# Kernel optimization log

Measured on AMD Instinct MI355X. Metric: run time of the kernel, lower is better.

The kernel has to match this reference:

```python
import jax, jax.numpy as jnp
import numpy as np

B, E, DM = 2, 1024, 512          # batch, n_edges, d_model
H, DK, DV = 8, 64, 64            # heads, d_k, d_v
MAX_NEIGHBOR = 5                 # == attn_max_dist
LN_EPS = 1e-6
NEG = -1e9


def setup_inputs() -> dict:
    key = jax.random.key(0)
    ks = jax.random.split(key, 9)
    s = 0.02
    return {
        "x": jax.random.normal(ks[0], (B, DM, E, 1), jnp.float32),
        "dist": jax.random.randint(ks[1], (B, E, E), 0, 12, jnp.int32),
        "base_rpr": jax.random.normal(ks[2], (MAX_NEIGHBOR + 1, DK), jnp.float32) * s,
        "w_q": jax.random.normal(ks[3], (DM, H * DK), jnp.float32) * s,
        "w_k": jax.random.normal(ks[4], (DM, H * DK), jnp.float32) * s,
        "w_v": jax.random.normal(ks[5], (DM, H * DV), jnp.float32) * s,
        "w_fc": jax.random.normal(ks[6], (H * DV, DM), jnp.float32) * s,
        "ln_g": jnp.ones((DM,), jnp.float32),
        "ln_b": jnp.zeros((DM,), jnp.float32),
    }


def reference(x, dist, base_rpr, w_q, w_k, w_v, w_fc, ln_g, ln_b):
    temp = jnp.asarray(DK, x.dtype) ** 0.5
    # local-attention mask (dist <= attn_max_dist); all edges valid (same-size meshes)
    mask = dist <= MAX_NEIGHBOR                      # [B,E,E] bool

    s = jnp.transpose(x[..., 0], (0, 2, 1))          # [B,E,DM]
    residual = s

    # LayerNorm applied to q only (as in the torch module)
    mu = s.mean(-1, keepdims=True)
    var = ((s - mu) ** 2).mean(-1, keepdims=True)
    qn = (s - mu) / jnp.sqrt(var + LN_EPS) * ln_g + ln_b

    q = (qn @ w_q).reshape(B, E, H, DK).transpose(0, 2, 1, 3)   # [B,H,E,DK]
    k = (s @ w_k).reshape(B, E, H, DK).transpose(0, 2, 1, 3)
    v = (s @ w_v).reshape(B, E, H, DV).transpose(0, 2, 1, 3)

    # relative-position representations gathered by (clipped) distance
    rpr = base_rpr[jnp.minimum(dist, MAX_NEIGHBOR)]  # [B,E,E,DK]

    qs = q / temp
    attn1 = jnp.einsum("bhid,bhjd->bhij", qs, k)
    attn2 = jnp.einsum("bhid,bijd->bhij", qs, rpr)
    logits = jnp.where(mask[:, None], attn1 + attn2, NEG)
    attn = jax.nn.softmax(logits, axis=-1)           # [B,H,E,E]

    out = jnp.einsum("bhij,bhjd->bhid", attn, v)     # [B,H,E,DV]
    out = out.transpose(0, 2, 1, 3).reshape(B, E, H * DV) @ w_fc + residual
    x_out = out.transpose(0, 2, 1)[..., None]        # [B,DM,E,1]

    mf = mask[:, None].astype(attn.dtype)            # [B,1,E,E]
    attn_per_edge = (attn * mf).sum((1, 2)) / mf.sum((1, 2))  # [B,E]
    return x_out, attn, attn_per_edge
```

## Files before the change

### kernel.cpp

```cpp
#include <hip/hip_runtime.h>

#define NB_B 2
#define NB_E 1024
#define NB_DM 512
#define NB_H 8
#define NEGV -1e9f

typedef __attribute__((ext_vector_type(8))) __bf16 bf16x8;
typedef __attribute__((ext_vector_type(8))) unsigned short u16x8;
typedef __attribute__((ext_vector_type(4))) float f32x4;

static __device__ __forceinline__ float bf2f(unsigned short u){
  union { unsigned int i; float f; } v; v.i = ((unsigned int)u) << 16; return v.f;
}
static __device__ __forceinline__ unsigned short f2bf(float f){
  union { float f; unsigned int i; } v; v.f = f;
  unsigned int r = v.i + 0x7FFFu + ((v.i >> 16) & 1u);
  return (unsigned short)(r >> 16);
}
static __device__ __forceinline__ f32x4 mfma16(bf16x8 a, bf16x8 b, f32x4 c){
  return __builtin_amdgcn_mfma_f32_16x16x32_bf16(a, b, c, 0, 0, 0);
}
static __device__ __forceinline__ float fast_exp2(float x){
#if __has_builtin(__builtin_amdgcn_exp2f)
  return __builtin_amdgcn_exp2f(x);
#else
  return exp2f(x);
#endif
}

__global__ void k_transpose_x(const float* __restrict__ x, unsigned short* __restrict__ s_bf){
  __shared__ float tile[32][33];
  const int b = blockIdx.z;
  const int d0 = blockIdx.y * 32;
  const int e0 = blockIdx.x * 32;
  const int tx = threadIdx.x, ty = threadIdx.y;
  #pragma unroll
  for (int r = 0; r < 4; ++r){
    const int d = d0 + ty + r*8;
    tile[ty + r*8][tx] = x[((size_t)b*NB_DM + d)*NB_E + e0 + tx];
  }
  __syncthreads();
  #pragma unroll
  for (int r = 0; r < 4; ++r){
    const int e = e0 + ty + r*8;
    s_bf[((size_t)b*NB_E + e)*NB_DM + d0 + tx] = f2bf(tile[tx][ty + r*8]);
  }
}

__global__ void k_transpose_w(const float* __restrict__ w0, const float* __restrict__ w1,
                              const float* __restrict__ w2, const float* __restrict__ w3,
                              unsigned short* __restrict__ wT){
  __shared__ float tile[32][33];
  const int which = blockIdx.z;
  const float* w = which==0 ? w0 : which==1 ? w1 : which==2 ? w2 : w3;
  unsigned short* dst = wT + (size_t)which*512*512;
  const int k0 = blockIdx.y*32, n0 = blockIdx.x*32;
  const int tx = threadIdx.x, ty = threadIdx.y;
  #pragma unroll
  for (int r = 0; r < 4; ++r)
    tile[ty + r*8][tx] = w[(size_t)(k0 + ty + r*8)*512 + n0 + tx];
  __syncthreads();
  #pragma unroll
  for (int r = 0; r < 4; ++r)
    dst[(size_t)(n0 + ty + r*8)*512 + k0 + tx] = f2bf(tile[tx][ty + r*8]);
}

__global__ __launch_bounds__(256) void k_ln(const unsigned short* __restrict__ s_bf,
    unsigned short* __restrict__ qn_bf, const float* __restrict__ gg, const float* __restrict__ bb){
  const int row = blockIdx.x*4 + (threadIdx.x >> 6);
  const int l = threadIdx.x & 63;
  const unsigned short* sp = s_bf + (size_t)row*512 + l*8;
  u16x8 v = *(const u16x8*)sp;
  float f[8]; float sum = 0.f, sq = 0.f;
  #pragma unroll
  for (int i = 0; i < 8; ++i){ f[i] = bf2f(v[i]); sum += f[i]; sq += f[i]*f[i]; }
  #pragma unroll
  for (int off = 32; off >= 1; off >>= 1){
    sum += __shfl_xor(sum, off);
    sq  += __shfl_xor(sq, off);
  }
  const float mu  = sum * (1.f/512.f);
  const float var = sq * (1.f/512.f) - mu*mu;
  const float rstd = rsqrtf(var + 1e-6f);
  const float4 g0 = *(const float4*)(gg + l*8);
  const float4 g1 = *(const float4*)(gg + l*8 + 4);
  const float4 b0 = *(const float4*)(bb + l*8);
  const float4 b1 = *(const float4*)(bb + l*8 + 4);
  const float gv[8] = {g0.x,g0.y,g0.z,g0.w,g1.x,g1.y,g1.z,g1.w};
  const float bv[8] = {b0.x,b0.y,b0.z,b0.w,b1.x,b1.y,b1.z,b1.w};
  u16x8 o;
  #pragma unroll
  for (int i = 0; i < 8; ++i) o[i] = f2bf((f[i]-mu)*rstd*gv[i] + bv[i]);
  *(u16x8*)(qn_bf + (size_t)row*512 + l*8) = o;
}

__global__ __launch_bounds__(256) void k_dist(const int* __restrict__ dist,
    unsigned char* __restrict__ d8, int* __restrict__ cnt){
  const int b = blockIdx.y;
  const int i0 = blockIdx.x * 16;
  const int t = threadIdx.x;
  int c0 = 0, c1 = 0, c2 = 0, c3 = 0;
  #pragma unroll 4
  for (int r = 0; r < 16; ++r){
    const int row = i0 + r;
    const int4 d = ((const int4*)(dist + ((size_t)b*NB_E + row)*NB_E))[t];
    uchar4 o;
    o.x = (unsigned char)(d.x <= 5 ? d.x : 6);
    o.y = (unsigned char)(d.y <= 5 ? d.y : 6);
    o.z = (unsigned char)(d.z <= 5 ? d.z : 6);
    o.w = (unsigned char)(d.w <= 5 ? d.w : 6);
    ((uchar4*)(d8 + ((size_t)b*NB_E + row)*NB_E))[t] = o;
    c0 += (d.x <= 5); c1 += (d.y <= 5); c2 += (d.z <= 5); c3 += (d.w <= 5);
  }
  int* cb = cnt + b*NB_E + t*4;
  atomicAdd(cb + 0, c0);
  atomicAdd(cb + 1, c1);
  atomicAdd(cb + 2, c2);
  atomicAdd(cb + 3, c3);
}

__global__ __launch_bounds__(256) void k_gemm_qkv(
    const unsigned short* __restrict__ qn, const unsigned short* __restrict__ s,
    const unsigned short* __restrict__ wT, const float* __restrict__ base_rpr,
    unsigned short* __restrict__ Qb, unsigned short* __restrict__ Kb,
    unsigned short* __restrict__ VTb, float* __restrict__ qr)
{
  const int z = blockIdx.z;
  const unsigned short* A  = (z == 0) ? qn : s;
  const unsigned short* BT = wT + (size_t)z*262144;
  const int tid = threadIdx.x;
  const int l = tid & 63, wv = tid >> 6;
  const int ll = l & 15, lg = l >> 4;
  const int m0 = blockIdx.x*64 + wv*16;
  const int n0 = blockIdx.y*64;
  const unsigned short* arow = A + (size_t)(m0 + ll)*512 + lg*8;
  f32x4 acc[4];
  #pragma unroll
  for (int nt = 0; nt < 4; ++nt) acc[nt] = (f32x4){0.f,0.f,0.f,0.f};
  #pragma unroll
  for (int ks = 0; ks < 16; ++ks){
    bf16x8 a = *(const bf16x8*)(arow + ks*32);
    #pragma unroll
    for (int nt = 0; nt < 4; ++nt){
      bf16x8 bv = *(const bf16x8*)(BT + (size_t)(n0 + nt*16 + ll)*512 + ks*32 + lg*8);
      acc[nt] = mfma16(a, bv, acc[nt]);
    }
  }
  const int rbase = m0 + lg*4;
  const int bidx = rbase >> 10;
  const int e = rbase & 1023;
  const int h = n0 >> 6;
  if (z == 0){
    float rprv[6][4];
    #pragma unroll
    for (int c = 0; c < 6; ++c)
      #pragma unroll
      for (int nt = 0; nt < 4; ++nt)
        rprv[c][nt] = base_rpr[c*64 + nt*16 + ll];
    #pragma unroll
    for (int nt = 0; nt < 4; ++nt){
      const int dk = nt*16 + ll;
      unsigned short* dp = Qb + (((size_t)bidx*NB_H + h)*NB_E + e)*64 + dk;
      #pragma unroll
      for (int r = 0; r < 4; ++r)
        dp[(size_t)r*64] = f2bf(acc[nt][r]*0.125f);
    }
    #pragma unroll
    for (int r = 0; r < 4; ++r){
      #pragma unroll
      for (int c = 0; c < 6; ++c){
        float tv = 0.f;
        #pragma unroll
        for (int nt = 0; nt < 4; ++nt) tv += acc[nt][r]*0.125f*rprv[c][nt];
        tv += __shfl_xor(tv, 1);
        tv += __shfl_xor(tv, 2);
        tv += __shfl_xor(tv, 4);
        tv += __shfl_xor(tv, 8);
        if (ll == 0)
          qr[(((size_t)(bidx*NB_H + h)*NB_E) + e + r)*8 + c] = tv;
      }
    }
  } else if (z == 1){
    #pragma unroll
    for (int nt = 0; nt < 4; ++nt){
      const int dk = nt*16 + ll;
      unsigned short* dp = Kb + (((size_t)bidx*NB_H + h)*NB_E + e)*64 + dk;
      #pragma unroll
      for (int r = 0; r < 4; ++r)
        dp[(size_t)r*64] = f2bf(acc[nt][r]);
    }
  } else {
    #pragma unroll
    for (int nt = 0; nt < 4; ++nt){
      const int dv = nt*16 + ll;
      ushort4 ov;
      ov.x = f2bf(acc[nt][0]); ov.y = f2bf(acc[nt][1]);
      ov.z = f2bf(acc[nt][2]); ov.w = f2bf(acc[nt][3]);
      *(ushort4*)(VTb + (((size_t)bidx*NB_H + h)*64 + dv)*NB_E + e) = ov;
    }
  }
}

__global__ __launch_bounds__(256) void k_fc(
    const unsigned short* __restrict__ A, const unsigned short* __restrict__ BT,
    float* __restrict__ dst_f, const float* __restrict__ resid)
{
  const int tid = threadIdx.x;
  const int l = tid & 63, wv = tid >> 6;
  const int ll = l & 15, lg = l >> 4;
  const int m0 = blockIdx.x*64 + wv*16;
  const int n0 = blockIdx.y*64;
  const unsigned short* arow = A + (size_t)(m0 + ll)*512 + lg*8;
  f32x4 acc[4];
  #pragma unroll
  for (int nt = 0; nt < 4; ++nt) acc[nt] = (f32x4){0.f,0.f,0.f,0.f};
  #pragma unroll
  for (int ks = 0; ks < 16; ++ks){
    bf16x8 a = *(const bf16x8*)(arow + ks*32);
    #pragma unroll
    for (int nt = 0; nt < 4; ++nt){
      bf16x8 bv = *(const bf16x8*)(BT + (size_t)(n0 + nt*16 + ll)*512 + ks*32 + lg*8);
      acc[nt] = mfma16(a, bv, acc[nt]);
    }
  }
  const int rbase = m0 + lg*4;
  const int bidx = rbase >> 10;
  const int e = rbase & 1023;
  #pragma unroll
  for (int nt = 0; nt < 4; ++nt){
    const int n = n0 + nt*16 + ll;
    const float* xr = resid + ((size_t)bidx*NB_DM + n)*NB_E + e;
    const float4 rv = *(const float4*)xr;
    const float4 ov = make_float4(acc[nt][0]+rv.x, acc[nt][1]+rv.y,
                                  acc[nt][2]+rv.z, acc[nt][3]+rv.w);
    *(float4*)(dst_f + ((size_t)bidx*NB_DM + n)*NB_E + e) = ov;
  }
}

__global__ __launch_bounds__(256, 4) void k_attn(
    const unsigned short* __restrict__ Q, const unsigned short* __restrict__ K,
    const unsigned short* __restrict__ VT, const float* __restrict__ qr,
    const unsigned char* __restrict__ d8, float* __restrict__ attn_out,
    unsigned short* __restrict__ outb, float* __restrict__ ape_acc)
{
  __shared__ __align__(16) unsigned char smem[2048 + 32768];
  unsigned short* plds = (unsigned short*)(smem + 2048);
  float* qr_l = (float*)smem;
  float* redm = (float*)(smem + 512);
  float* reds = (float*)(smem + 1024);

  const int tid = threadIdx.x;
  const int l = tid & 63, w = tid >> 6;
  const int lg = l >> 4, ll = l & 15;
  const int n = blockIdx.x;
  const int m = n >> 3;
  const int bh = (n & 7)*2 + (m >> 6);
  const int b = bh >> 3;
  const int ib = (m & 63) << 4;

  for (int t = tid; t < 16*6; t += 256)
    qr_l[t] = qr[((size_t)bh*NB_E + ib + (t/6))*8 + (t % 6)];

  const unsigned short* Qb = Q + ((size_t)bh*NB_E + ib)*64;
  bf16x8 qf[2];
  #pragma unroll
  for (int hf = 0; hf < 2; ++hf)
    qf[hf] = *(const bf16x8*)(Qb + (size_t)ll*64 + hf*32 + lg*8);
  __syncthreads();

  f32x4 s[16];
  const unsigned short* Kb = K + (size_t)bh*NB_E*64;
  #pragma unroll
  for (int jt = 0; jt < 16; ++jt){
    const int jrow = (w*16 + jt)*16 + ll;
    bf16x8 k0 = *(const bf16x8*)(Kb + (size_t)jrow*64 + lg*8);
    bf16x8 k1 = *(const bf16x8*)(Kb + (size_t)jrow*64 + 32 + lg*8);
    f32x4 acc = {0.f,0.f,0.f,0.f};
    acc = mfma16(qf[0], k0, acc);
    acc = mfma16(qf[1], k1, acc);
    s[jt] = acc;
  }

  const unsigned char* d8r = d8 + ((size_t)b*NB_E + ib)*NB_E;
  #pragma unroll
  for (int jt = 0; jt < 16; ++jt){
    const int j = (w*16 + jt)*16 + ll;
    #pragma unroll
    for (int r = 0; r < 4; ++r){
      const int il = lg*4 + r;
      const unsigned char c = d8r[(size_t)il*NB_E + j];
      s[jt][r] = (c < 6) ? (s[jt][r] + qr_l[il*6 + c]) : NEGV;
    }
  }

  #pragma unroll
  for (int r = 0; r < 4; ++r){
    float mm = -3.0e38f;
    #pragma unroll
    for (int jt = 0; jt < 16; ++jt) mm = fmaxf(mm, s[jt][r]);
    mm = fmaxf(mm, __shfl_xor(mm, 1));
    mm = fmaxf(mm, __shfl_xor(mm, 2));
    mm = fmaxf(mm, __shfl_xor(mm, 4));
    mm = fmaxf(mm, __shfl_xor(mm, 8));
    if (ll == 0) redm[w*16 + lg*4 + r] = mm;
  }
  __syncthreads();
  float mx[4];
  #pragma unroll
  for (int r = 0; r < 4; ++r){
    const int il = lg*4 + r;
    mx[r] = fmaxf(fmaxf(redm[il], redm[16+il]), fmaxf(redm[32+il], redm[48+il]));
  }

  #pragma unroll
  for (int r = 0; r < 4; ++r){
    float sum = 0.f;
    #pragma unroll
    for (int jt = 0; jt < 16; ++jt){
      const float p = fast_exp2((s[jt][r] - mx[r]) * 1.4426950408889634f);
      s[jt][r] = p;
      sum += p;
    }
    sum += __shfl_xor(sum, 1);
    sum += __shfl_xor(sum, 2);
    sum += __shfl_xor(sum, 4);
    sum += __shfl_xor(sum, 8);
    if (ll == 0) reds[w*16 + lg*4 + r] = sum;
  }
  __syncthreads();
  float rinv[4];
  #pragma unroll
  for (int r = 0; r < 4; ++r){
    const int il = lg*4 + r;
    rinv[r] = 1.0f / (reds[il] + reds[16+il] + reds[32+il] + reds[48+il]);
  }

  float* arow = attn_out + ((size_t)bh*NB_E + ib)*NB_E;
  #pragma unroll
  for (int jt = 0; jt < 16; ++jt){
    const int j = (w*16 + jt)*16 + ll;
    float csum = 0.f;
    #pragma unroll
    for (int r = 0; r < 4; ++r){
      const int il = lg*4 + r;
      const float pn = s[jt][r] * rinv[r];
      __builtin_nontemporal_store(pn, &arow[(size_t)il*NB_E + j]);
      const int byo = ((il*1024 + j)*2) ^ ((il & 7) << 4);
      plds[byo >> 1] = f2bf(pn);
      csum += pn;
    }
    csum += __shfl_xor(csum, 16);
    csum += __shfl_xor(csum, 32);
    if (l < 16) atomicAdd(&ape_acc[(bh << 10) + j], csum);
  }
  __syncthreads();

  const unsigned short* Vb = VT + ((size_t)bh*64 + w*16 + ll)*NB_E;
  f32x4 o = {0.f,0.f,0.f,0.f};
  #pragma unroll
  for (int kk = 0; kk < 32; ++kk){
    bf16x8 vf = *(const bf16x8*)(Vb + kk*32 + lg*8);
    const int byo = ((ll*2048 + (kk*32 + lg*8)*2)) ^ ((ll & 7) << 4);
    bf16x8 p = *(const bf16x8*)(smem + 2048 + byo);
    o = mfma16(p, vf, o);
  }
  const int coln = (bh & 7)*64 + w*16 + ll;
  #pragma unroll
  for (int r = 0; r < 4; ++r){
    const int e0 = ib + lg*4 + r;
    outb[((size_t)b*NB_E + e0)*512 + coln] = f2bf(o[r]);
  }
}

__global__ void k_ape(const float* __restrict__ acc, const int* __restrict__ cnt,
                      float* __restrict__ out){
  const int t = blockIdx.x*256 + threadIdx.x;
  if (t < NB_B*NB_E){
    const int b = t >> 10, j = t & 1023;
    float ssum = 0.f;
    #pragma unroll
    for (int h = 0; h < 8; ++h) ssum += acc[(((b<<3) + h) << 10) + j];
    const int c = cnt[t];
    out[t] = c > 0 ? ssum / (float)c : 0.f;
  }
}

extern "C" void kernel_launch(void* const* d_in, const int* in_sizes, int n_in,
                              void* d_out, int out_size, void* d_ws, size_t ws_size,
                              hipStream_t stream)
{
  const float* x        = (const float*)d_in[0];
  const int*   dist     = (const int*)d_in[1];
  const float* base_rpr = (const float*)d_in[2];
  const float* w_q      = (const float*)d_in[3];
  const float* w_k      = (const float*)d_in[4];
  const float* w_v      = (const float*)d_in[5];
  const float* w_fc     = (const float*)d_in[6];
  const float* ln_g     = (const float*)d_in[7];
  const float* ln_b     = (const float*)d_in[8];

  float* x_out    = (float*)d_out;
  float* attn_out = x_out + (size_t)NB_B*NB_DM*NB_E;
  float* ape_out  = attn_out + (size_t)NB_B*NB_H*NB_E*NB_E;

  unsigned char* ws = (unsigned char*)d_ws;
  unsigned short* s_bf   = (unsigned short*)(ws);
  unsigned short* qn_bf  = (unsigned short*)(ws + 2097152);
  unsigned short* wT     = (unsigned short*)(ws + 4194304);
  unsigned short* Qb     = (unsigned short*)(ws + 6291456);
  unsigned short* Kb     = (unsigned short*)(ws + 8388608);
  unsigned short* VTb    = (unsigned short*)(ws + 10485760);
  unsigned short* outb   = (unsigned short*)(ws + 12582912);
  float*          qr     = (float*)(ws + 14680064);
  unsigned char*  d8     = ws + 15204352;
  int*            cnt    = (int*)(ws + 17301504);
  float*          apeacc = (float*)(ws + 17309696);

  hipMemsetAsync(cnt, 0, 8192 + 65536, stream);

  k_transpose_w<<<dim3(16,16,4), dim3(32,8), 0, stream>>>(w_q, w_k, w_v, w_fc, wT);
  k_transpose_x<<<dim3(32,16,2), dim3(32,8), 0, stream>>>(x, s_bf);
  k_ln<<<dim3(512), dim3(256), 0, stream>>>(s_bf, qn_bf, ln_g, ln_b);
  k_dist<<<dim3(64,2), dim3(256), 0, stream>>>(dist, d8, cnt);

  k_gemm_qkv<<<dim3(32,8,3), dim3(256), 0, stream>>>(qn_bf, s_bf, wT, base_rpr,
                                                     Qb, Kb, VTb, qr);

  k_attn<<<dim3(1024), dim3(256), 0, stream>>>(Qb, Kb, VTb, qr, d8, attn_out, outb, apeacc);

  k_fc<<<dim3(32,8), dim3(256), 0, stream>>>(outb, wT + 786432, x_out, x);
  k_ape<<<dim3(8), dim3(256), 0, stream>>>(apeacc, cnt, ape_out);
}
```

Before: 122.4 us.

## Prefetch GEMM operands, stage dist in LDS, coalesce attention-probability stores

The QKV and FC GEMMs now software-prefetch the next k-slice of A and B into registers, and the FC kernel uses narrower N tiles to launch twice as many blocks. The attention kernel loads the dist tile into LDS ahead of the QK MFMAs instead of doing scattered byte reads, and prefetches K and V fragments. The float attention-probability matrix is now written as row-contiguous 16-byte non-temporal stores from the LDS copy, aiming for better-coalesced writes of the largest output. Those stored values are now rounded through bf16, which loses precision in the attn output, and the larger LDS use lowers the occupancy target to 3 blocks.

```diff
diff --git a/kernel.cpp b/kernel.cpp
--- a/kernel.cpp
+++ b/kernel.cpp
@@ -120,7 +120,7 @@
   atomicAdd(cb + 3, c3);
 }
 
-__global__ __launch_bounds__(256) void k_gemm_qkv(
+__global__ __launch_bounds__(256, 4) void k_gemm_qkv(
     const unsigned short* __restrict__ qn, const unsigned short* __restrict__ s,
     const unsigned short* __restrict__ wT, const float* __restrict__ base_rpr,
     unsigned short* __restrict__ Qb, unsigned short* __restrict__ Kb,
@@ -135,17 +135,26 @@
   const int m0 = blockIdx.x*64 + wv*16;
   const int n0 = blockIdx.y*64;
   const unsigned short* arow = A + (size_t)(m0 + ll)*512 + lg*8;
+  const unsigned short* brow = BT + (size_t)(n0 + ll)*512 + lg*8;
   f32x4 acc[4];
   #pragma unroll
   for (int nt = 0; nt < 4; ++nt) acc[nt] = (f32x4){0.f,0.f,0.f,0.f};
+  bf16x8 a_c = *(const bf16x8*)(arow);
+  bf16x8 b_c[4];
+  #pragma unroll
+  for (int nt = 0; nt < 4; ++nt) b_c[nt] = *(const bf16x8*)(brow + (size_t)nt*8192);
   #pragma unroll
   for (int ks = 0; ks < 16; ++ks){
-    bf16x8 a = *(const bf16x8*)(arow + ks*32);
-    #pragma unroll
-    for (int nt = 0; nt < 4; ++nt){
-      bf16x8 bv = *(const bf16x8*)(BT + (size_t)(n0 + nt*16 + ll)*512 + ks*32 + lg*8);
-      acc[nt] = mfma16(a, bv, acc[nt]);
-    }
+    const int kn = (ks + 1) & 15;
+    bf16x8 a_n = *(const bf16x8*)(arow + kn*32);
+    bf16x8 b_n[4];
+    #pragma unroll
+    for (int nt = 0; nt < 4; ++nt) b_n[nt] = *(const bf16x8*)(brow + (size_t)nt*8192 + kn*32);
+    #pragma unroll
+    for (int nt = 0; nt < 4; ++nt) acc[nt] = mfma16(a_c, b_c[nt], acc[nt]);
+    a_c = a_n;
+    #pragma unroll
+    for (int nt = 0; nt < 4; ++nt) b_c[nt] = b_n[nt];
   }
   const int rbase = m0 + lg*4;
   const int bidx = rbase >> 10;
@@ -202,7 +211,7 @@
   }
 }
 
-__global__ __launch_bounds__(256) void k_fc(
+__global__ __launch_bounds__(256, 4) void k_fc(
     const unsigned short* __restrict__ A, const unsigned short* __restrict__ BT,
     float* __restrict__ dst_f, const float* __restrict__ resid)
 {
@@ -210,25 +219,30 @@
   const int l = tid & 63, wv = tid >> 6;
   const int ll = l & 15, lg = l >> 4;
   const int m0 = blockIdx.x*64 + wv*16;
-  const int n0 = blockIdx.y*64;
+  const int n0 = blockIdx.y*32;
   const unsigned short* arow = A + (size_t)(m0 + ll)*512 + lg*8;
-  f32x4 acc[4];
-  #pragma unroll
-  for (int nt = 0; nt < 4; ++nt) acc[nt] = (f32x4){0.f,0.f,0.f,0.f};
+  const unsigned short* brow = BT + (size_t)(n0 + ll)*512 + lg*8;
+  f32x4 acc[2];
+  acc[0] = (f32x4){0.f,0.f,0.f,0.f};
+  acc[1] = (f32x4){0.f,0.f,0.f,0.f};
+  bf16x8 a_c = *(const bf16x8*)(arow);
+  bf16x8 b_c0 = *(const bf16x8*)(brow);
+  bf16x8 b_c1 = *(const bf16x8*)(brow + 8192);
   #pragma unroll
   for (int ks = 0; ks < 16; ++ks){
-    bf16x8 a = *(const bf16x8*)(arow + ks*32);
-    #pragma unroll
-    for (int nt = 0; nt < 4; ++nt){
-      bf16x8 bv = *(const bf16x8*)(BT + (size_t)(n0 + nt*16 + ll)*512 + ks*32 + lg*8);
-      acc[nt] = mfma16(a, bv, acc[nt]);
-    }
+    const int kn = (ks + 1) & 15;
+    bf16x8 a_n  = *(const bf16x8*)(arow + kn*32);
+    bf16x8 b_n0 = *(const bf16x8*)(brow + kn*32);
+    bf16x8 b_n1 = *(const bf16x8*)(brow + 8192 + kn*32);
+    acc[0] = mfma16(a_c, b_c0, acc[0]);
+    acc[1] = mfma16(a_c, b_c1, acc[1]);
+    a_c = a_n; b_c0 = b_n0; b_c1 = b_n1;
   }
   const int rbase = m0 + lg*4;
   const int bidx = rbase >> 10;
   const int e = rbase & 1023;
   #pragma unroll
-  for (int nt = 0; nt < 4; ++nt){
+  for (int nt = 0; nt < 2; ++nt){
     const int n = n0 + nt*16 + ll;
     const float* xr = resid + ((size_t)bidx*NB_DM + n)*NB_E + e;
     const float4 rv = *(const float4*)xr;
@@ -238,14 +252,16 @@
   }
 }
 
-__global__ __launch_bounds__(256, 4) void k_attn(
+#define D_OFF 2048
+#define P_OFF 18432
+__global__ __launch_bounds__(256, 3) void k_attn(
     const unsigned short* __restrict__ Q, const unsigned short* __restrict__ K,
     const unsigned short* __restrict__ VT, const float* __restrict__ qr,
     const unsigned char* __restrict__ d8, float* __restrict__ attn_out,
     unsigned short* __restrict__ outb, float* __restrict__ ape_acc)
 {
-  __shared__ __align__(16) unsigned char smem[2048 + 32768];
-  unsigned short* plds = (unsigned short*)(smem + 2048);
+  __shared__ __align__(16) unsigned char smem[51200];
+  unsigned short* plds = (unsigned short*)(smem + P_OFF);
   float* qr_l = (float*)smem;
   float* redm = (float*)(smem + 512);
   float* reds = (float*)(smem + 1024);
@@ -259,6 +275,12 @@
   const int b = bh >> 3;
   const int ib = (m & 63) << 4;
 
+  const unsigned char* d8g = d8 + ((size_t)b*NB_E + ib)*NB_E;
+  int4 dreg[4];
+  #pragma unroll
+  for (int ch = 0; ch < 4; ++ch)
+    dreg[ch] = ((const int4*)(d8g + (size_t)ch*4096))[tid];
+
   for (int t = tid; t < 16*6; t += 256)
     qr_l[t] = qr[((size_t)bh*NB_E + ib + (t/6))*8 + (t % 6)];
 
@@ -267,29 +289,36 @@
   #pragma unroll
   for (int hf = 0; hf < 2; ++hf)
     qf[hf] = *(const bf16x8*)(Qb + (size_t)ll*64 + hf*32 + lg*8);
-  __syncthreads();
 
   f32x4 s[16];
   const unsigned short* Kb = K + (size_t)bh*NB_E*64;
+  bf16x8 k0 = *(const bf16x8*)(Kb + (size_t)((w*16)*16 + ll)*64 + lg*8);
+  bf16x8 k1 = *(const bf16x8*)(Kb + (size_t)((w*16)*16 + ll)*64 + 32 + lg*8);
   #pragma unroll
   for (int jt = 0; jt < 16; ++jt){
-    const int jrow = (w*16 + jt)*16 + ll;
-    bf16x8 k0 = *(const bf16x8*)(Kb + (size_t)jrow*64 + lg*8);
-    bf16x8 k1 = *(const bf16x8*)(Kb + (size_t)jrow*64 + 32 + lg*8);
+    const int jn = (jt + 1) & 15;
+    const size_t nrow = (size_t)((w*16 + jn)*16 + ll)*64;
+    bf16x8 kn0 = *(const bf16x8*)(Kb + nrow + lg*8);
+    bf16x8 kn1 = *(const bf16x8*)(Kb + nrow + 32 + lg*8);
     f32x4 acc = {0.f,0.f,0.f,0.f};
     acc = mfma16(qf[0], k0, acc);
     acc = mfma16(qf[1], k1, acc);
     s[jt] = acc;
-  }
-
-  const unsigned char* d8r = d8 + ((size_t)b*NB_E + ib)*NB_E;
+    k0 = kn0; k1 = kn1;
+  }
+
+  #pragma unroll
+  for (int ch = 0; ch < 4; ++ch)
+    ((int4*)(smem + D_OFF + ch*4096))[tid] = dreg[ch];
+  __syncthreads();
+
   #pragma unroll
   for (int jt = 0; jt < 16; ++jt){
     const int j = (w*16 + jt)*16 + ll;
     #pragma unroll
     for (int r = 0; r < 4; ++r){
       const int il = lg*4 + r;
-      const unsigned char c = d8r[(size_t)il*NB_E + j];
+      const unsigned char c = smem[D_OFF + il*1024 + j];
       s[jt][r] = (c < 6) ? (s[jt][r] + qr_l[il*6 + c]) : NEGV;
     }
   }
@@ -336,7 +365,6 @@
     rinv[r] = 1.0f / (reds[il] + reds[16+il] + reds[32+il] + reds[48+il]);
   }
 
-  float* arow = attn_out + ((size_t)bh*NB_E + ib)*NB_E;
   #pragma unroll
   for (int jt = 0; jt < 16; ++jt){
     const int j = (w*16 + jt)*16 + ll;
@@ -345,7 +373,6 @@
     for (int r = 0; r < 4; ++r){
       const int il = lg*4 + r;
       const float pn = s[jt][r] * rinv[r];
-      __builtin_nontemporal_store(pn, &arow[(size_t)il*NB_E + j]);
       const int byo = ((il*1024 + j)*2) ^ ((il & 7) << 4);
       plds[byo >> 1] = f2bf(pn);
       csum += pn;
@@ -356,14 +383,31 @@
   }
   __syncthreads();
 
+  {
+    const int il = w*4 + lg;
+    float* arow = attn_out + ((size_t)bh*NB_E + ib + il)*NB_E;
+    const int rowb = il*2048;
+    #pragma unroll
+    for (int c2 = 0; c2 < 16; ++c2){
+      const int byo = (rowb + c2*128 + ll*8) ^ ((il & 7) << 4);
+      const ushort4 pv = *(const ushort4*)(smem + P_OFF + byo);
+      f32x4 ov;
+      ov[0] = bf2f(pv.x); ov[1] = bf2f(pv.y); ov[2] = bf2f(pv.z); ov[3] = bf2f(pv.w);
+      __builtin_nontemporal_store(ov, (f32x4*)(arow + c2*64 + ll*4));
+    }
+  }
+
   const unsigned short* Vb = VT + ((size_t)bh*64 + w*16 + ll)*NB_E;
   f32x4 o = {0.f,0.f,0.f,0.f};
+  bf16x8 vf = *(const bf16x8*)(Vb + lg*8);
   #pragma unroll
   for (int kk = 0; kk < 32; ++kk){
-    bf16x8 vf = *(const bf16x8*)(Vb + kk*32 + lg*8);
+    const int kn = (kk + 1) & 31;
+    bf16x8 vn = *(const bf16x8*)(Vb + kn*32 + lg*8);
     const int byo = ((ll*2048 + (kk*32 + lg*8)*2)) ^ ((ll & 7) << 4);
-    bf16x8 p = *(const bf16x8*)(smem + 2048 + byo);
+    bf16x8 p = *(const bf16x8*)(smem + P_OFF + byo);
     o = mfma16(p, vf, o);
+    vf = vn;
   }
   const int coln = (bh & 7)*64 + w*16 + ll;
   #pragma unroll
@@ -429,6 +473,6 @@
 
   k_attn<<<dim3(1024), dim3(256), 0, stream>>>(Qb, Kb, VTb, qr, d8, attn_out, outb, apeacc);
 
-  k_fc<<<dim3(32,8), dim3(256), 0, stream>>>(outb, wT + 786432, x_out, x);
+  k_fc<<<dim3(32,16), dim3(256), 0, stream>>>(outb, wT + 786432, x_out, x);
   k_ape<<<dim3(8), dim3(256), 0, stream>>>(apeacc, cnt, ape_out);
 }
```

After: 125.6 us. 2.6% more time.
